# Performance work log

Measured on AMD Instinct MI355X. Metric: run time of the kernel, lower is better.

Reference implementation:

```python
import jax, jax.numpy as jnp
import numpy as np

N = 50000      # nodes
E = 800000     # edges (before self-loops)
IN = 512       # input_dim
ENC = 256      # encoding_dim
HID = 32       # hidden_dim per head
HEADS = 4
OUT = 40       # output_dim (classes)
SLOPE = 0.2    # PyG GATConv negative_slope default


def setup_inputs() -> dict:
    key = jax.random.key(0)
    ks = jax.random.split(key, 14)
    w = lambda k, shape: jax.random.normal(k, shape, jnp.float32) * 0.02
    return {
        "x": jax.random.normal(ks[0], (N, IN), jnp.float32),
        "edge_index": jax.random.randint(ks[1], (2, E), 0, N, jnp.int64),
        # Autoencoder (fc3 unused in its forward)
        "ae_w1": w(ks[2], (IN, ENC)), "ae_b1": jnp.zeros((ENC,), jnp.float32),
        "ae_w2": w(ks[3], (ENC, ENC)), "ae_b2": jnp.zeros((ENC,), jnp.float32),
        # GAT layer 1: ENC -> HID per head, HEADS heads, concat
        "gat1_w": w(ks[4], (ENC, HEADS * HID)),
        "gat1_att_src": w(ks[5], (HEADS, HID)),
        "gat1_att_dst": w(ks[6], (HEADS, HID)),
        "gat1_b": jnp.zeros((HEADS * HID,), jnp.float32),
        # GAT layer 2: HEADS*HID -> OUT, 1 head, no concat (mean)
        "gat2_w": w(ks[7], (HEADS * HID, OUT)),
        "gat2_att_src": w(ks[8], (1, OUT)),
        "gat2_att_dst": w(ks[9], (1, OUT)),
        "gat2_b": jnp.zeros((OUT,), jnp.float32),
        # Residual dense branches
        "res1_w": w(ks[10], (ENC, HEADS * HID)), "res1_b": jnp.zeros((HEADS * HID,), jnp.float32),
        "res2_w": w(ks[11], (HEADS * HID, OUT)), "res2_b": jnp.zeros((OUT,), jnp.float32),
    }


def _gat_conv(x, W, att_src, att_dst, bias, src, dst, heads, ch, concat):
    # x: [N, F_in] -> h: [N, heads, ch]
    h = (x @ W).reshape(-1, heads, ch)
    a_src = jnp.sum(h * att_src, axis=-1)   # [N, heads]
    a_dst = jnp.sum(h * att_dst, axis=-1)   # [N, heads]
    e = jax.nn.leaky_relu(a_src[src] + a_dst[dst], SLOPE)  # [E, heads]
    # segment softmax over edges grouped by target node
    m = jax.ops.segment_max(e, dst, num_segments=N)        # [N, heads]
    ee = jnp.exp(e - m[dst])
    den = jax.ops.segment_sum(ee, dst, num_segments=N)
    alpha = ee / jnp.maximum(den[dst], 1e-16)              # [E, heads]
    out = jax.ops.segment_sum(h[src] * alpha[..., None], dst, num_segments=N)  # [N, heads, ch]
    out = out.reshape(-1, heads * ch) if concat else out.mean(axis=1)
    return out + bias


def reference(x, edge_index, ae_w1, ae_b1, ae_w2, ae_b2,
              gat1_w, gat1_att_src, gat1_att_dst, gat1_b,
              gat2_w, gat2_att_src, gat2_att_dst, gat2_b,
              res1_w, res1_b, res2_w, res2_b):
    # add self-loops (PyG GATConv default)
    loops = jnp.arange(N, dtype=edge_index.dtype)
    src = jnp.concatenate([edge_index[0], loops])
    dst = jnp.concatenate([edge_index[1], loops])

    # autoencoder encode (fc1, fc2 only)
    xe = jax.nn.relu(jax.nn.relu(x @ ae_w1 + ae_b1) @ ae_w2 + ae_b2)

    g1 = _gat_conv(xe, gat1_w, gat1_att_src, gat1_att_dst, gat1_b, src, dst, HEADS, HID, True)
    h = jax.nn.relu(g1 + xe @ res1_w + res1_b)

    g2 = _gat_conv(h, gat2_w, gat2_att_src, gat2_att_dst, gat2_b, src, dst, 1, OUT, False)
    return g2 + h @ res2_w + res2_b
```

## Files before the change

kernel.cpp:

```cpp
#include <hip/hip_runtime.h>
#include <hip/hip_bf16.h>
#include <math.h>

#define HEADS 4
#define OUTC 40
#define SLOPE 0.2f

typedef __attribute__((ext_vector_type(8))) short bf16x8;
typedef __attribute__((ext_vector_type(4))) float f32x4;

__device__ __forceinline__ short f2bf(float f) {
    unsigned u = __float_as_uint(f);
    unsigned r = (u + 0x7FFFu + ((u >> 16) & 1u)) >> 16;
    return (short)r;
}
__device__ __forceinline__ float bf2f(short s) {
    return __uint_as_float(((unsigned)(unsigned short)s) << 16);
}
__device__ __forceinline__ float bfu2f(unsigned short s) {
    return __uint_as_float(((unsigned)s) << 16);
}

typedef const __attribute__((address_space(1))) unsigned int gu32;
typedef __attribute__((address_space(3))) unsigned int lu32;
__device__ __forceinline__ void gll16(const void* src, void* lds) {
    __builtin_amdgcn_global_load_lds((gu32*)src, (lu32*)lds, 16, 0, 0);
}

template<int BM_, int AMODE, int EPI, int FUSE>
__global__ __launch_bounds__(256) void gemm2(
    const float* __restrict__ Af,
    const short* __restrict__ A,
    const short* __restrict__ B,
    const float* __restrict__ bias,
    unsigned short* __restrict__ Obf, unsigned short* __restrict__ Ob2,
    float* __restrict__ Of,
    int M, int N, int K,
    const int* __restrict__ fA, const int* __restrict__ fB,
    const int* __restrict__ fC, const int* __restrict__ fD,
    int* __restrict__ fX, int* __restrict__ fY_,
    int fE, int fN, int fy)
{
    if (FUSE == 1 && (int)blockIdx.y >= fy) {
        int e = ((blockIdx.y - fy) * gridDim.x + blockIdx.x) * 256 + threadIdx.x;
        if (e < fE) fY_[e] = atomicAdd(&fX[fA[e]], 1);
        return;
    }
    if (FUSE == 2 && (int)blockIdx.y >= fy) {
        int e = ((blockIdx.y - fy) * gridDim.x + blockIdx.x) * 256 + threadIdx.x;
        if (e < fE) {
            fX[fD[fB[e]] + fC[e]] = fA[e];
        } else if (e < fE + fN) {
            int n = e - fE;
            fX[fD[n + 1] - 1] = n;
        }
        return;
    }

    constexpr int MI = BM_ / 32;
    __shared__ short smem[BM_ * 64 + 8192];
    short* As = smem;
    short* Bs = smem + BM_ * 64;

    const int tid = threadIdx.x;
    const int wid = tid >> 6, lane = tid & 63;
    const int bm = blockIdx.y * BM_, bn = blockIdx.x * 128;
    const int wm = wid >> 1, wn = wid & 1;
    const int rA = lane & 15, kb = lane >> 4;

    f32x4 acc[MI][4];
    #pragma unroll
    for (int i = 0; i < MI; i++)
        #pragma unroll
        for (int j = 0; j < 4; j++)
            acc[i][j] = (f32x4){0.f, 0.f, 0.f, 0.f};

    const int KT = K >> 6;

    const float* asrcF[BM_ / 32];
    #pragma unroll
    for (int it = 0; it < BM_ / 32; it++) {
        int g = it * 256 + tid;
        int row = g >> 3, gr = g & 7;
        int gsrc = gr ^ (row & 7);
        int grow = bm + row; if (grow > M - 1) grow = M - 1;
        asrcF[it] = AMODE ? (Af + (size_t)grow * K + gsrc * 8) : nullptr;
    }

    f32x4 pf0[BM_ / 32], pf1[BM_ / 32];

    auto LOADA = [&](int kt) {
        #pragma unroll
        for (int it = 0; it < BM_ / 32; it++) {
            const float* s = asrcF[it] + ((size_t)kt << 6);
            pf0[it] = *(const f32x4*)s;
            pf1[it] = *(const f32x4*)(s + 4);
        }
    };
    auto STAGE_A_REG = [&]() {
        #pragma unroll
        for (int it = 0; it < BM_ / 32; it++) {
            bf16x8 v;
            v[0] = f2bf(pf0[it][0]); v[1] = f2bf(pf0[it][1]);
            v[2] = f2bf(pf0[it][2]); v[3] = f2bf(pf0[it][3]);
            v[4] = f2bf(pf1[it][0]); v[5] = f2bf(pf1[it][1]);
            v[6] = f2bf(pf1[it][2]); v[7] = f2bf(pf1[it][3]);
            *(bf16x8*)(As + (size_t)(it * 256 + tid) * 8) = v;
        }
    };
    auto STAGE_A_LDS = [&](int kt) {
        const int k0 = kt << 6;
        #pragma unroll
        for (int it = 0; it < BM_ / 32; it++) {
            int g = it * 256 + tid;
            int row = g >> 3, gr = g & 7;
            int gsrc = gr ^ (row & 7);
            int grow = bm + row; if (grow > M - 1) grow = M - 1;
            gll16(A + (size_t)grow * K + k0 + gsrc * 8,
                  As + (it * 256 + wid * 64) * 8);
        }
    };
    auto STAGE_B = [&](int kt) {
        const int k0 = kt << 6;
        #pragma unroll
        for (int it = 0; it < 4; it++) {
            int g = it * 256 + tid;
            int row = g >> 3, gr = g & 7;
            int gsrc = gr ^ (row & 7);
            gll16(B + (size_t)(bn + row) * K + k0 + gsrc * 8,
                  Bs + (it * 256 + wid * 64) * 8);
        }
    };
    auto COMPUTE = [&]() {
        #pragma unroll
        for (int kc = 0; kc < 2; kc++) {
            bf16x8 a[MI], b[4];
            #pragma unroll
            for (int mi = 0; mi < MI; mi++) {
                int r = wm * (BM_ / 2) + mi * 16 + rA;
                int off = r * 64 + (((kc * 4 + kb) ^ (r & 7)) * 8);
                a[mi] = *(const bf16x8*)(As + off);
            }
            #pragma unroll
            for (int ni = 0; ni < 4; ni++) {
                int r = wn * 64 + ni * 16 + rA;
                int off = r * 64 + (((kc * 4 + kb) ^ (r & 7)) * 8);
                b[ni] = *(const bf16x8*)(Bs + off);
            }
            #pragma unroll
            for (int mi = 0; mi < MI; mi++)
                #pragma unroll
                for (int ni = 0; ni < 4; ni++)
                    acc[mi][ni] = __builtin_amdgcn_mfma_f32_16x16x32_bf16(a[mi], b[ni], acc[mi][ni], 0, 0, 0);
        }
    };

    if (AMODE == 1) LOADA(0);
    for (int kt = 0; kt < KT; kt++) {
        if (AMODE == 0) STAGE_A_LDS(kt); else STAGE_A_REG();
        STAGE_B(kt);
        __syncthreads();
        if (AMODE == 1 && kt + 1 < KT) LOADA(kt + 1);
        COMPUTE();
        __syncthreads();
    }

    #pragma unroll
    for (int ni = 0; ni < 4; ni++) {
        int col = bn + wn * 64 + ni * 16 + rA;
        float bv = (EPI == 0) ? bias[col] : 0.f;
        #pragma unroll
        for (int mi = 0; mi < MI; mi++) {
            #pragma unroll
            for (int j = 0; j < 4; j++) {
                int row = bm + wm * (BM_ / 2) + mi * 16 + kb * 4 + j;
                if (row < M) {
                    float v = acc[mi][ni][j];
                    if (EPI == 0) {
                        v = fmaxf(v + bv, 0.f);
                        Obf[(size_t)row * N + col] = (unsigned short)f2bf(v);
                    } else if (EPI == 1) {
                        if (col < 128) Obf[(size_t)row * 128 + col] = (unsigned short)f2bf(v);
                        else           Ob2[(size_t)row * 128 + (col - 128)] = (unsigned short)f2bf(v);
                    } else {
                        if (col < 80) {
                            v += bias[col];
                            Of[(size_t)row * 80 + col] = v;
                            if (col < OUTC)
                                Obf[(size_t)row * OUTC + col] = (unsigned short)f2bf(v);
                        }
                    }
                }
            }
        }
    }
}

__global__ void wprep(const float* __restrict__ ae_w1, const float* __restrict__ ae_w2,
                      const float* __restrict__ g1w, const float* __restrict__ r1w,
                      const float* __restrict__ g2w, const float* __restrict__ r2w,
                      const float* __restrict__ r2b,
                      short* __restrict__ w1T, short* __restrict__ w2T,
                      short* __restrict__ wc1, short* __restrict__ wc2T,
                      float* __restrict__ cb2) {
    int gid = blockIdx.x * blockDim.x + threadIdx.x;
    if (gid < 131072) {
        int n = gid >> 9, k = gid & 511;
        w1T[gid] = f2bf(ae_w1[(size_t)k * 256 + n]);
        return;
    }
    gid -= 131072;
    if (gid < 65536) {
        int n = gid >> 8, k = gid & 255;
        w2T[gid] = f2bf(ae_w2[(size_t)k * 256 + n]);
        return;
    }
    gid -= 65536;
    if (gid < 65536) {
        int n = gid >> 8, k = gid & 255;
        float v = (n < 128) ? g1w[(size_t)k * 128 + n] : r1w[(size_t)k * 128 + (n - 128)];
        wc1[gid] = f2bf(v);
        return;
    }
    gid -= 65536;
    if (gid < 16384) {
        int n = gid >> 7, k = gid & 127;
        float v = 0.f;
        if (n < OUTC)          v = g2w[k * OUTC + n];
        else if (n < 2 * OUTC) v = r2w[k * OUTC + (n - OUTC)];
        wc2T[gid] = f2bf(v);
        return;
    }
    gid -= 16384;
    if (gid < 80) cb2[gid] = (gid < OUTC) ? 0.f : r2b[gid - OUTC];
}

__global__ void scan_part(const int* __restrict__ deg, int N, int* __restrict__ part) {
    __shared__ int s[256];
    int b = blockIdx.x, t = threadIdx.x;
    int i0 = b * 1024 + t * 4;
    int sum = 0;
    #pragma unroll
    for (int j = 0; j < 4; j++) { int i = i0 + j; if (i < N) sum += deg[i] + 1; }
    s[t] = sum; __syncthreads();
    for (int o = 128; o; o >>= 1) { if (t < o) s[t] += s[t + o]; __syncthreads(); }
    if (t == 0) part[b] = s[0];
}

__global__ void scan_base(int* __restrict__ part, int nb, int* __restrict__ offs) {
    int t = threadIdx.x;
    int v = (t < nb) ? part[t] : 0;
    int v0 = v;
    for (int o = 1; o < 64; o <<= 1) {
        int u = __shfl_up(v, o, 64);
        if (t >= o) v += u;
    }
    if (t < nb) part[t] = v - v0;
    if (t == 0) offs[0] = 0;
}

__global__ void scan_final(const int* __restrict__ deg, int N, const int* __restrict__ part,
                           int* __restrict__ offs) {
    __shared__ int s[256];
    int b = blockIdx.x, t = threadIdx.x;
    int i0 = b * 1024 + t * 4;
    int v[4]; int sum = 0;
    #pragma unroll
    for (int j = 0; j < 4; j++) { int i = i0 + j; v[j] = (i < N) ? deg[i] + 1 : 0; sum += v[j]; }
    s[t] = sum; __syncthreads();
    for (int o = 1; o < 256; o <<= 1) {
        int add = (t >= o) ? s[t - o] : 0;
        __syncthreads();
        s[t] += add;
        __syncthreads();
    }
    int excl = s[t] - sum + part[b];
    #pragma unroll
    for (int j = 0; j < 4; j++) {
        int i = i0 + j;
        if (i < N) { offs[i + 1] = excl + v[j]; excl += v[j]; }
    }
}

__global__ void att1(const unsigned short* __restrict__ h1b, const float* __restrict__ atts,
                     const float* __restrict__ attd, float* __restrict__ as1,
                     float* __restrict__ ad1, int N) {
    int idx = blockIdx.x * blockDim.x + threadIdx.x;
    if (idx >= N * HEADS) return;
    int n = idx >> 2, h = idx & 3;
    const unsigned short* row = h1b + (size_t)n * 128 + h * 32;
    float ss = 0.f, dd = 0.f;
    #pragma unroll
    for (int c4 = 0; c4 < 4; c4++) {
        uint4 v = *(const uint4*)(row + c4 * 8);
        float4 ws1 = *(const float4*)(atts + h * 32 + c4 * 8);
        float4 ws2 = *(const float4*)(atts + h * 32 + c4 * 8 + 4);
        float4 wd1 = *(const float4*)(attd + h * 32 + c4 * 8);
        float4 wd2 = *(const float4*)(attd + h * 32 + c4 * 8 + 4);
        float e0 = bfu2f((unsigned short)(v.x & 0xFFFF)), e1 = bfu2f((unsigned short)(v.x >> 16));
        float e2 = bfu2f((unsigned short)(v.y & 0xFFFF)), e3 = bfu2f((unsigned short)(v.y >> 16));
        float e4 = bfu2f((unsigned short)(v.z & 0xFFFF)), e5 = bfu2f((unsigned short)(v.z >> 16));
        float e6 = bfu2f((unsigned short)(v.w & 0xFFFF)), e7 = bfu2f((unsigned short)(v.w >> 16));
        ss += e0*ws1.x + e1*ws1.y + e2*ws1.z + e3*ws1.w + e4*ws2.x + e5*ws2.y + e6*ws2.z + e7*ws2.w;
        dd += e0*wd1.x + e1*wd1.y + e2*wd1.z + e3*wd1.w + e4*wd2.x + e5*wd2.y + e6*wd2.z + e7*wd2.w;
    }
    as1[idx] = ss; ad1[idx] = dd;
}

__global__ void att2(const float* __restrict__ h2r2, const float* __restrict__ atts,
                     const float* __restrict__ attd, float* __restrict__ as2,
                     float* __restrict__ ad2, int N) {
    int n = blockIdx.x * blockDim.x + threadIdx.x;
    if (n >= N) return;
    const float* row = h2r2 + (size_t)n * 80;
    float ss = 0.f, dd = 0.f;
    #pragma unroll
    for (int c = 0; c < OUTC; c += 4) {
        float4 v = *(const float4*)(row + c);
        float4 ws = *(const float4*)(atts + c);
        float4 wd = *(const float4*)(attd + c);
        ss += v.x*ws.x + v.y*ws.y + v.z*ws.z + v.w*ws.w;
        dd += v.x*wd.x + v.y*wd.y + v.z*wd.z + v.w*wd.w;
    }
    as2[n] = ss; ad2[n] = dd;
}

__global__ __launch_bounds__(256) void maxden1(const float* __restrict__ as1,
                                               const float* __restrict__ ad1,
                                               const int* __restrict__ offs,
                                               const int* __restrict__ csr,
                                               float* __restrict__ va,
                                               float* __restrict__ m1,
                                               float* __restrict__ invden1, int N) {
    int n = blockIdx.x * 4 + (threadIdx.x >> 6);
    if (n >= N) return;
    int t = threadIdx.x & 63;
    int h = t >> 4, l = t & 15;
    int beg = offs[n], d = offs[n + 1] - beg;
    float adst = ad1[n * 4 + h];
    float mx = -INFINITY;
    for (int j = l; j < d; j += 16) {
        int idx = beg + j;
        int s = csr[idx];
        float v = as1[s * 4 + h] + adst;
        v = v >= 0.f ? v : SLOPE * v;
        va[(size_t)idx * 4 + h] = v;
        mx = fmaxf(mx, v);
    }
    #pragma unroll
    for (int o = 8; o; o >>= 1) mx = fmaxf(mx, __shfl_xor(mx, o, 16));
    float den = 0.f;
    for (int j = l; j < d; j += 16) {
        den += __expf(va[(size_t)(beg + j) * 4 + h] - mx);
    }
    #pragma unroll
    for (int o = 8; o; o >>= 1) den += __shfl_xor(den, o, 16);
    if (l == 0) {
        m1[n * 4 + h] = mx;
        invden1[n * 4 + h] = 1.f / fmaxf(den, 1e-16f);
    }
}

__global__ __launch_bounds__(256) void maxden2(const float* __restrict__ as2,
                                               const float* __restrict__ ad2,
                                               const int* __restrict__ offs,
                                               const int* __restrict__ csr,
                                               float* __restrict__ va,
                                               float* __restrict__ m2,
                                               float* __restrict__ invden2, int N) {
    int n = blockIdx.x * 4 + (threadIdx.x >> 6);
    if (n >= N) return;
    int t = threadIdx.x & 63;
    int beg = offs[n], d = offs[n + 1] - beg;
    float adst = ad2[n];
    float mx = -INFINITY;
    for (int j = t; j < d; j += 64) {
        int idx = beg + j;
        int s = csr[idx];
        float v = as2[s] + adst;
        v = v >= 0.f ? v : SLOPE * v;
        va[idx] = v;
        mx = fmaxf(mx, v);
    }
    #pragma unroll
    for (int o = 32; o; o >>= 1) mx = fmaxf(mx, __shfl_xor(mx, o, 64));
    float den = 0.f;
    for (int j = t; j < d; j += 64) {
        den += __expf(va[beg + j] - mx);
    }
    #pragma unroll
    for (int o = 32; o; o >>= 1) den += __shfl_xor(den, o, 64);
    if (t == 0) {
        m2[n] = mx;
        invden2[n] = 1.f / fmaxf(den, 1e-16f);
    }
}

__global__ __launch_bounds__(256) void gat1_agg(const unsigned short* __restrict__ h1b,
                                                const unsigned short* __restrict__ r1b,
                                                const float* __restrict__ va,
                                                const float* __restrict__ m1,
                                                const float* __restrict__ iv1,
                                                const int* __restrict__ offs,
                                                const int* __restrict__ csr,
                                                const float* __restrict__ gb,
                                                const float* __restrict__ rb,
                                                unsigned short* __restrict__ hbufb, int N) {
    int n = blockIdx.x * 4 + (threadIdx.x >> 6);
    if (n >= N) return;
    int t = threadIdx.x & 63;
    int h = t >> 4;
    int beg = offs[n], d = offs[n + 1] - beg;
    float m = m1[n * 4 + h];
    float iv = iv1[n * 4 + h];

    float acc0 = 0.f, acc1 = 0.f;
    int s[8]; float w[8];
    #pragma unroll
    for (int u = 0; u < 8; u++) {
        bool ok = u < d;
        int idx = beg + (ok ? u : 0);
        s[u] = ok ? csr[idx] : 0;
        w[u] = ok ? va[(size_t)idx * 4 + h] : -1e30f;
    }
    for (int j = 0; j < d; j += 8) {
        int cs[8]; float cw[8];
        #pragma unroll
        for (int u = 0; u < 8; u++) { cs[u] = s[u]; cw[u] = __expf(w[u] - m); }
        #pragma unroll
        for (int u = 0; u < 8; u++) {
            int jj = j + 8 + u;
            bool ok = jj < d;
            int idx = beg + (ok ? jj : 0);
            s[u] = ok ? csr[idx] : 0;
            w[u] = ok ? va[(size_t)idx * 4 + h] : -1e30f;
        }
        #pragma unroll
        for (int u = 0; u < 8; u++) {
            ushort2 hv = *(const ushort2*)(h1b + (size_t)cs[u] * 128 + 2 * t);
            acc0 += cw[u] * bfu2f(hv.x);
            acc1 += cw[u] * bfu2f(hv.y);
        }
    }
    acc0 *= iv; acc1 *= iv;
    ushort2 rv = *(const ushort2*)(r1b + (size_t)n * 128 + 2 * t);
    float2 gv = *(const float2*)(gb + 2 * t);
    float2 bv = *(const float2*)(rb + 2 * t);
    float o0 = fmaxf(acc0 + gv.x + bv.x + bfu2f(rv.x), 0.f);
    float o1 = fmaxf(acc1 + gv.y + bv.y + bfu2f(rv.y), 0.f);
    ushort2 ov = {(unsigned short)f2bf(o0), (unsigned short)f2bf(o1)};
    *(ushort2*)(hbufb + (size_t)n * 128 + 2 * t) = ov;
}

__global__ __launch_bounds__(256) void gat2_agg(const unsigned short* __restrict__ h2b,
                                                const float* __restrict__ h2r2,
                                                const float* __restrict__ va,
                                                const float* __restrict__ m2,
                                                const float* __restrict__ iv2,
                                                const int* __restrict__ offs,
                                                const int* __restrict__ csr,
                                                const float* __restrict__ gb,
                                                float* __restrict__ out, int N) {
    int n = blockIdx.x * 4 + (threadIdx.x >> 6);
    if (n >= N) return;
    int t = threadIdx.x & 63;
    int beg = offs[n], d = offs[n + 1] - beg;
    float m = m2[n];
    float iv = iv2[n];

    float acc0 = 0.f, acc1 = 0.f;
    int s[8]; float w[8];
    #pragma unroll
    for (int u = 0; u < 8; u++) {
        bool ok = u < d;
        int idx = beg + (ok ? u : 0);
        s[u] = ok ? csr[idx] : 0;
        w[u] = ok ? va[idx] : -1e30f;
    }
    for (int j = 0; j < d; j += 8) {
        int cs[8]; float cw[8];
        #pragma unroll
        for (int u = 0; u < 8; u++) { cs[u] = s[u]; cw[u] = __expf(w[u] - m); }
        #pragma unroll
        for (int u = 0; u < 8; u++) {
            int jj = j + 8 + u;
            bool ok = jj < d;
            int idx = beg + (ok ? jj : 0);
            s[u] = ok ? csr[idx] : 0;
            w[u] = ok ? va[idx] : -1e30f;
        }
        if (t < 20) {
            #pragma unroll
            for (int u = 0; u < 8; u++) {
                ushort2 hv = *(const ushort2*)(h2b + (size_t)cs[u] * OUTC + 2 * t);
                acc0 += cw[u] * bfu2f(hv.x);
                acc1 += cw[u] * bfu2f(hv.y);
            }
        }
    }
    if (t < 20) {
        float2 rr = *(const float2*)(h2r2 + (size_t)n * 80 + 40 + 2 * t);
        float2 gv = *(const float2*)(gb + 2 * t);
        float2 ov = {acc0 * iv + gv.x + rr.x, acc1 * iv + gv.y + rr.y};
        *(float2*)(out + (size_t)n * OUTC + 2 * t) = ov;
    }
}

extern "C" void kernel_launch(void* const* d_in, const int* in_sizes, int n_in,
                              void* d_out, int out_size, void* d_ws, size_t ws_size,
                              hipStream_t stream) {
    const float* x      = (const float*)d_in[0];
    const int*   ei     = (const int*)d_in[1];
    const float* ae_w1  = (const float*)d_in[2];
    const float* ae_b1  = (const float*)d_in[3];
    const float* ae_w2  = (const float*)d_in[4];
    const float* ae_b2  = (const float*)d_in[5];
    const float* gat1_w = (const float*)d_in[6];
    const float* g1as   = (const float*)d_in[7];
    const float* g1ad   = (const float*)d_in[8];
    const float* g1b    = (const float*)d_in[9];
    const float* gat2_w = (const float*)d_in[10];
    const float* g2as   = (const float*)d_in[11];
    const float* g2ad   = (const float*)d_in[12];
    const float* g2b    = (const float*)d_in[13];
    const float* res1_w = (const float*)d_in[14];
    const float* res1_b = (const float*)d_in[15];
    const float* res2_w = (const float*)d_in[16];
    const float* res2_b = (const float*)d_in[17];
    float* out = (float*)d_out;

    const int Nn = in_sizes[0] / 512;
    const int E  = in_sizes[1] / 2;
    const int Etot = E + Nn;

    const int* srcA = ei;
    const int* dstA = ei + E;

    char* W = (char*)d_ws;
    size_t off = 0;
    auto alloc = [&](size_t bytes) { char* p = W + off; off += (bytes + 255) & ~(size_t)255; return p; };

    unsigned short* y1b   = (unsigned short*)alloc((size_t)Nn * 256 * 2);
    unsigned short* xeb   = (unsigned short*)alloc((size_t)Nn * 256 * 2);
    unsigned short* h1b   = (unsigned short*)alloc((size_t)Nn * 128 * 2);
    unsigned short* r1b   = (unsigned short*)alloc((size_t)Nn * 128 * 2);
    unsigned short* hbufb = (unsigned short*)alloc((size_t)Nn * 128 * 2);
    float*          h2r2  = (float*)alloc((size_t)Nn * 80 * 4);
    unsigned short* h2bf  = (unsigned short*)alloc((size_t)Nn * OUTC * 2);

    short* w1T  = (short*)alloc(256 * 512 * 2);
    short* w2T  = (short*)alloc(256 * 256 * 2);
    short* wc1  = (short*)alloc(256 * 256 * 2);
    short* wc2T = (short*)alloc(128 * 128 * 2);
    float* cb2  = (float*)alloc(80 * 4);
    float* as1  = (float*)alloc((size_t)Nn * HEADS * 4);
    float* ad1  = (float*)alloc((size_t)Nn * HEADS * 4);
    float* as2  = (float*)alloc((size_t)Nn * 4);
    float* ad2  = (float*)alloc((size_t)Nn * 4);
    float* m1   = (float*)alloc((size_t)Nn * HEADS * 4);
    float* iv1  = (float*)alloc((size_t)Nn * HEADS * 4);
    float* m2   = (float*)alloc((size_t)Nn * 4);
    float* iv2  = (float*)alloc((size_t)Nn * 4);
    float* va1  = (float*)alloc((size_t)Etot * HEADS * 4);
    float* va2  = (float*)alloc((size_t)Etot * 4);
    int* deg  = (int*)alloc((size_t)Nn * 4);
    int* offs = (int*)alloc((size_t)(Nn + 1) * 4);
    int* rank = (int*)alloc((size_t)E * 4);
    int* part = (int*)alloc(256 * 4);
    int* csr  = (int*)alloc((size_t)Etot * 4);

    {
        int total = 131072 + 65536 + 65536 + 16384 + 80;
        wprep<<<(total + 255) / 256, 256, 0, stream>>>(
            ae_w1, ae_w2, gat1_w, res1_w, gat2_w, res2_w, res2_b,
            w1T, w2T, wc1, wc2T, cb2);
    }
    hipMemsetAsync(deg, 0, (size_t)Nn * sizeof(int), stream);

    const int gy1 = (Nn + 31) / 32;
    const int gy2 = (Nn + 63) / 64;
    const int cntRows  = (E + 511) / 512;
    const int scatRows = (E + Nn + 511) / 512;

    gemm2<32, 1, 0, 1><<<dim3(2, gy1 + cntRows), 256, 0, stream>>>(
        x, nullptr, w1T, ae_b1, y1b, nullptr, nullptr, Nn, 256, 512,
        dstA, nullptr, nullptr, nullptr, deg, rank, E, 0, gy1);

    int nb = (Nn + 1023) / 1024;
    scan_part<<<nb, 256, 0, stream>>>(deg, Nn, part);
    scan_base<<<1, 64, 0, stream>>>(part, nb, offs);
    scan_final<<<nb, 256, 0, stream>>>(deg, Nn, part, offs);

    gemm2<64, 0, 0, 2><<<dim3(2, gy2 + scatRows), 256, 0, stream>>>(
        nullptr, (const short*)y1b, w2T, ae_b2, xeb, nullptr, nullptr, Nn, 256, 256,
        srcA, dstA, rank, offs, csr, nullptr, E, Nn, gy2);

    gemm2<64, 0, 1, 0><<<dim3(2, gy2), 256, 0, stream>>>(
        nullptr, (const short*)xeb, wc1, nullptr, h1b, r1b, nullptr, Nn, 256, 256,
        nullptr, nullptr, nullptr, nullptr, nullptr, nullptr, 0, 0, 0);

    att1<<<(Nn * HEADS + 255) / 256, 256, 0, stream>>>(h1b, g1as, g1ad, as1, ad1, Nn);
    maxden1<<<(Nn + 3) / 4, 256, 0, stream>>>(as1, ad1, offs, csr, va1, m1, iv1, Nn);
    gat1_agg<<<(Nn + 3) / 4, 256, 0, stream>>>(h1b, r1b, va1, m1, iv1, offs, csr, g1b, res1_b, hbufb, Nn);

    gemm2<64, 0, 2, 0><<<dim3(1, gy2), 256, 0, stream>>>(
        nullptr, (const short*)hbufb, wc2T, cb2, h2bf, nullptr, h2r2, Nn, 128, 128,
        nullptr, nullptr, nullptr, nullptr, nullptr, nullptr, 0, 0, 0);

    att2<<<(Nn + 255) / 256, 256, 0, stream>>>(h2r2, g2as, g2ad, as2, ad2, Nn);
    maxden2<<<(Nn + 3) / 4, 256, 0, stream>>>(as2, ad2, offs, csr, va2, m2, iv2, Nn);
    gat2_agg<<<(Nn + 3) / 4, 256, 0, stream>>>(h2bf, h2r2, va2, m2, iv2, offs, csr, g2b, out, Nn);
}
```

Baseline: 274.7 us.

## Fuse softmax max/denominator passes into GAT aggregation kernels using LDS score cache

Merges the separate max/denominator kernels into the aggregation kernels for both GAT layers. Per-edge leaky-relu scores and source indices are kept in shared memory, up to 128 edges per node, with a recompute fallback for higher-degree nodes. This removes the global per-edge score buffers, the max and inverse-denominator arrays, and two kernel launches. The cost is losing the register prefetch pipeline in the gather loop, plus relying on intra-wavefront LDS visibility without an explicit barrier.

```diff
diff --git a/kernel.cpp b/kernel.cpp
--- a/kernel.cpp
+++ b/kernel.cpp
@@ -5,6 +5,7 @@
 #define HEADS 4
 #define OUTC 40
 #define SLOPE 0.2f
+#define DCAP 128
 
 typedef __attribute__((ext_vector_type(8))) short bf16x8;
 typedef __attribute__((ext_vector_type(4))) float f32x4;
@@ -325,115 +326,69 @@
     as2[n] = ss; ad2[n] = dd;
 }
 
-__global__ __launch_bounds__(256) void maxden1(const float* __restrict__ as1,
-                                               const float* __restrict__ ad1,
-                                               const int* __restrict__ offs,
-                                               const int* __restrict__ csr,
-                                               float* __restrict__ va,
-                                               float* __restrict__ m1,
-                                               float* __restrict__ invden1, int N) {
-    int n = blockIdx.x * 4 + (threadIdx.x >> 6);
+__global__ __launch_bounds__(256) void gat1_fused(const unsigned short* __restrict__ h1b,
+                                                  const unsigned short* __restrict__ r1b,
+                                                  const float* __restrict__ as1,
+                                                  const float* __restrict__ ad1,
+                                                  const int* __restrict__ offs,
+                                                  const int* __restrict__ csr,
+                                                  const float* __restrict__ gb,
+                                                  const float* __restrict__ rb,
+                                                  unsigned short* __restrict__ hbufb, int N) {
+    __shared__ float sc[4][DCAP * 4];
+    __shared__ int  scs[4][DCAP];
+    int nl = threadIdx.x >> 6;
+    int n = blockIdx.x * 4 + nl;
     if (n >= N) return;
     int t = threadIdx.x & 63;
     int h = t >> 4, l = t & 15;
     int beg = offs[n], d = offs[n + 1] - beg;
     float adst = ad1[n * 4 + h];
+
     float mx = -INFINITY;
     for (int j = l; j < d; j += 16) {
-        int idx = beg + j;
-        int s = csr[idx];
+        int s = csr[beg + j];
         float v = as1[s * 4 + h] + adst;
         v = v >= 0.f ? v : SLOPE * v;
-        va[(size_t)idx * 4 + h] = v;
+        if (j < DCAP) {
+            sc[nl][j * 4 + h] = v;
+            if (h == 0) scs[nl][j] = s;
+        }
         mx = fmaxf(mx, v);
     }
     #pragma unroll
     for (int o = 8; o; o >>= 1) mx = fmaxf(mx, __shfl_xor(mx, o, 16));
     float den = 0.f;
     for (int j = l; j < d; j += 16) {
-        den += __expf(va[(size_t)(beg + j) * 4 + h] - mx);
+        float v;
+        if (j < DCAP) v = sc[nl][j * 4 + h];
+        else {
+            int s = csr[beg + j];
+            v = as1[s * 4 + h] + adst;
+            v = v >= 0.f ? v : SLOPE * v;
+        }
+        den += __expf(v - mx);
     }
     #pragma unroll
     for (int o = 8; o; o >>= 1) den += __shfl_xor(den, o, 16);
-    if (l == 0) {
-        m1[n * 4 + h] = mx;
-        invden1[n * 4 + h] = 1.f / fmaxf(den, 1e-16f);
-    }
-}
-
-__global__ __launch_bounds__(256) void maxden2(const float* __restrict__ as2,
-                                               const float* __restrict__ ad2,
-                                               const int* __restrict__ offs,
-                                               const int* __restrict__ csr,
-                                               float* __restrict__ va,
-                                               float* __restrict__ m2,
-                                               float* __restrict__ invden2, int N) {
-    int n = blockIdx.x * 4 + (threadIdx.x >> 6);
-    if (n >= N) return;
-    int t = threadIdx.x & 63;
-    int beg = offs[n], d = offs[n + 1] - beg;
-    float adst = ad2[n];
-    float mx = -INFINITY;
-    for (int j = t; j < d; j += 64) {
-        int idx = beg + j;
-        int s = csr[idx];
-        float v = as2[s] + adst;
-        v = v >= 0.f ? v : SLOPE * v;
-        va[idx] = v;
-        mx = fmaxf(mx, v);
-    }
-    #pragma unroll
-    for (int o = 32; o; o >>= 1) mx = fmaxf(mx, __shfl_xor(mx, o, 64));
-    float den = 0.f;
-    for (int j = t; j < d; j += 64) {
-        den += __expf(va[beg + j] - mx);
-    }
-    #pragma unroll
-    for (int o = 32; o; o >>= 1) den += __shfl_xor(den, o, 64);
-    if (t == 0) {
-        m2[n] = mx;
-        invden2[n] = 1.f / fmaxf(den, 1e-16f);
-    }
-}
-
-__global__ __launch_bounds__(256) void gat1_agg(const unsigned short* __restrict__ h1b,
-                                                const unsigned short* __restrict__ r1b,
-                                                const float* __restrict__ va,
-                                                const float* __restrict__ m1,
-                                                const float* __restrict__ iv1,
-                                                const int* __restrict__ offs,
-                                                const int* __restrict__ csr,
-                                                const float* __restrict__ gb,
-                                                const float* __restrict__ rb,
-                                                unsigned short* __restrict__ hbufb, int N) {
-    int n = blockIdx.x * 4 + (threadIdx.x >> 6);
-    if (n >= N) return;
-    int t = threadIdx.x & 63;
-    int h = t >> 4;
-    int beg = offs[n], d = offs[n + 1] - beg;
-    float m = m1[n * 4 + h];
-    float iv = iv1[n * 4 + h];
+    float iv = 1.f / fmaxf(den, 1e-16f);
 
     float acc0 = 0.f, acc1 = 0.f;
-    int s[8]; float w[8];
-    #pragma unroll
-    for (int u = 0; u < 8; u++) {
-        bool ok = u < d;
-        int idx = beg + (ok ? u : 0);
-        s[u] = ok ? csr[idx] : 0;
-        w[u] = ok ? va[(size_t)idx * 4 + h] : -1e30f;
-    }
     for (int j = 0; j < d; j += 8) {
         int cs[8]; float cw[8];
         #pragma unroll
-        for (int u = 0; u < 8; u++) { cs[u] = s[u]; cw[u] = __expf(w[u] - m); }
-        #pragma unroll
         for (int u = 0; u < 8; u++) {
-            int jj = j + 8 + u;
-            bool ok = jj < d;
-            int idx = beg + (ok ? jj : 0);
-            s[u] = ok ? csr[idx] : 0;
-            w[u] = ok ? va[(size_t)idx * 4 + h] : -1e30f;
+            int jj = j + u;
+            if (jj < d && jj < DCAP) {
+                cs[u] = scs[nl][jj];
+                cw[u] = __expf(sc[nl][jj * 4 + h] - mx);
+            } else if (jj < d) {
+                int s = csr[beg + jj];
+                cs[u] = s;
+                float v = as1[s * 4 + h] + adst;
+                v = v >= 0.f ? v : SLOPE * v;
+                cw[u] = __expf(v - mx);
+            } else { cs[u] = 0; cw[u] = 0.f; }
         }
         #pragma unroll
         for (int u = 0; u < 8; u++) {
@@ -452,42 +407,64 @@
     *(ushort2*)(hbufb + (size_t)n * 128 + 2 * t) = ov;
 }
 
-__global__ __launch_bounds__(256) void gat2_agg(const unsigned short* __restrict__ h2b,
-                                                const float* __restrict__ h2r2,
-                                                const float* __restrict__ va,
-                                                const float* __restrict__ m2,
-                                                const float* __restrict__ iv2,
-                                                const int* __restrict__ offs,
-                                                const int* __restrict__ csr,
-                                                const float* __restrict__ gb,
-                                                float* __restrict__ out, int N) {
-    int n = blockIdx.x * 4 + (threadIdx.x >> 6);
+__global__ __launch_bounds__(256) void gat2_fused(const unsigned short* __restrict__ h2b,
+                                                  const float* __restrict__ h2r2,
+                                                  const float* __restrict__ as2,
+                                                  const float* __restrict__ ad2,
+                                                  const int* __restrict__ offs,
+                                                  const int* __restrict__ csr,
+                                                  const float* __restrict__ gb,
+                                                  float* __restrict__ out, int N) {
+    __shared__ float sc[4][DCAP];
+    __shared__ int  scs[4][DCAP];
+    int nl = threadIdx.x >> 6;
+    int n = blockIdx.x * 4 + nl;
     if (n >= N) return;
     int t = threadIdx.x & 63;
     int beg = offs[n], d = offs[n + 1] - beg;
-    float m = m2[n];
-    float iv = iv2[n];
+    float adst = ad2[n];
+
+    float mx = -INFINITY;
+    for (int j = t; j < d; j += 64) {
+        int s = csr[beg + j];
+        float v = as2[s] + adst;
+        v = v >= 0.f ? v : SLOPE * v;
+        if (j < DCAP) { sc[nl][j] = v; scs[nl][j] = s; }
+        mx = fmaxf(mx, v);
+    }
+    #pragma unroll
+    for (int o = 32; o; o >>= 1) mx = fmaxf(mx, __shfl_xor(mx, o, 64));
+    float den = 0.f;
+    for (int j = t; j < d; j += 64) {
+        float v;
+        if (j < DCAP) v = sc[nl][j];
+        else {
+            int s = csr[beg + j];
+            v = as2[s] + adst;
+            v = v >= 0.f ? v : SLOPE * v;
+        }
+        den += __expf(v - mx);
+    }
+    #pragma unroll
+    for (int o = 32; o; o >>= 1) den += __shfl_xor(den, o, 64);
+    float iv = 1.f / fmaxf(den, 1e-16f);
 
     float acc0 = 0.f, acc1 = 0.f;
-    int s[8]; float w[8];
-    #pragma unroll
-    for (int u = 0; u < 8; u++) {
-        bool ok = u < d;
-        int idx = beg + (ok ? u : 0);
-        s[u] = ok ? csr[idx] : 0;
-        w[u] = ok ? va[idx] : -1e30f;
-    }
     for (int j = 0; j < d; j += 8) {
         int cs[8]; float cw[8];
         #pragma unroll
-        for (int u = 0; u < 8; u++) { cs[u] = s[u]; cw[u] = __expf(w[u] - m); }
-        #pragma unroll
         for (int u = 0; u < 8; u++) {
-            int jj = j + 8 + u;
-            bool ok = jj < d;
-            int idx = beg + (ok ? jj : 0);
-            s[u] = ok ? csr[idx] : 0;
-            w[u] = ok ? va[idx] : -1e30f;
+            int jj = j + u;
+            if (jj < d && jj < DCAP) {
+                cs[u] = scs[nl][jj];
+                cw[u] = __expf(sc[nl][jj] - mx);
+            } else if (jj < d) {
+                int s = csr[beg + jj];
+                cs[u] = s;
+                float v = as2[s] + adst;
+                v = v >= 0.f ? v : SLOPE * v;
+                cw[u] = __expf(v - mx);
+            } else { cs[u] = 0; cw[u] = 0.f; }
         }
         if (t < 20) {
             #pragma unroll
@@ -557,12 +534,6 @@
     float* ad1  = (float*)alloc((size_t)Nn * HEADS * 4);
     float* as2  = (float*)alloc((size_t)Nn * 4);
     float* ad2  = (float*)alloc((size_t)Nn * 4);
-    float* m1   = (float*)alloc((size_t)Nn * HEADS * 4);
-    float* iv1  = (float*)alloc((size_t)Nn * HEADS * 4);
-    float* m2   = (float*)alloc((size_t)Nn * 4);
-    float* iv2  = (float*)alloc((size_t)Nn * 4);
-    float* va1  = (float*)alloc((size_t)Etot * HEADS * 4);
-    float* va2  = (float*)alloc((size_t)Etot * 4);
     int* deg  = (int*)alloc((size_t)Nn * 4);
     int* offs = (int*)alloc((size_t)(Nn + 1) * 4);
     int* rank = (int*)alloc((size_t)E * 4);
@@ -600,14 +571,12 @@
         nullptr, nullptr, nullptr, nullptr, nullptr, nullptr, 0, 0, 0);
 
     att1<<<(Nn * HEADS + 255) / 256, 256, 0, stream>>>(h1b, g1as, g1ad, as1, ad1, Nn);
-    maxden1<<<(Nn + 3) / 4, 256, 0, stream>>>(as1, ad1, offs, csr, va1, m1, iv1, Nn);
-    gat1_agg<<<(Nn + 3) / 4, 256, 0, stream>>>(h1b, r1b, va1, m1, iv1, offs, csr, g1b, res1_b, hbufb, Nn);
+    gat1_fused<<<(Nn + 3) / 4, 256, 0, stream>>>(h1b, r1b, as1, ad1, offs, csr, g1b, res1_b, hbufb, Nn);
 
     gemm2<64, 0, 2, 0><<<dim3(1, gy2), 256, 0, stream>>>(
         nullptr, (const short*)hbufb, wc2T, cb2, h2bf, nullptr, h2r2, Nn, 128, 128,
         nullptr, nullptr, nullptr, nullptr, nullptr, nullptr, 0, 0, 0);
 
     att2<<<(Nn + 255) / 256, 256, 0, stream>>>(h2r2, g2as, g2ad, as2, ad2, Nn);
-    maxden2<<<(Nn + 3) / 4, 256, 0, stream>>>(as2, ad2, offs, csr, va2, m2, iv2, Nn);
-    gat2_agg<<<(Nn + 3) / 4, 256, 0, stream>>>(h2bf, h2r2, va2, m2, iv2, offs, csr, g2b, out, Nn);
-}
+    gat2_fused<<<(Nn + 3) / 4, 256, 0, stream>>>(h2bf, h2r2, as2, ad2, offs, csr, g2b, out, Nn);
+}
```

Result: faster. 239.8 us (-12.7%).
